# Optimization experiments

Measured on AMD Instinct MI355X. Metric: run time of the kernel, lower is better.

Reference implementation:

```python
import jax, jax.numpy as jnp
import numpy as np
import math

B, S, D = 16, 1024, 512
ALPHA = 1.0
DIRECTION = 'fw'


def masked_softmax(vec, mask):
    # faithful to the torch helper: multiply-by-mask, max-shift, exp, re-mask, normalize
    masked_vec = vec * mask
    max_vec = jnp.max(masked_vec, axis=2, keepdims=True)
    exps = jnp.exp(masked_vec - max_vec)
    masked_exps = exps * mask
    masked_sums = jnp.sum(masked_exps, axis=2, keepdims=True)
    masked_sums = masked_sums + (masked_sums == 0).astype(vec.dtype)
    return masked_exps / (masked_sums + 1e-20)


def setup_inputs() -> dict:
    key = jax.random.key(0)
    kq, kk, kv, km = jax.random.split(key, 4)
    q = jax.random.normal(kq, (B, S, D), dtype=jnp.float32)
    k = jax.random.normal(kk, (B, S, D), dtype=jnp.float32)
    v = jax.random.normal(kv, (B, S, D), dtype=jnp.float32)
    rep_mask = jax.random.randint(km, (B, S, 1), 0, 2, dtype=jnp.int32)
    return {"q": q, "k": k, "v": v, "rep_mask": rep_mask}


def reference(q, k, v, rep_mask):
    seq_len = q.shape[1]
    scale = jnp.asarray(math.sqrt(D), dtype=q.dtype)
    attention = jnp.einsum('bqd,bkd->bqk', q, k) / scale  # [B,S,S]

    ones = jnp.ones((seq_len, seq_len), dtype=q.dtype)
    if DIRECTION == 'fw':
        dir_mask = jnp.tril(ones, k=-1)
    else:
        dir_mask = jnp.triu(ones, k=1)

    rm = rep_mask.astype(q.dtype)                     # [B,S,1]
    rep = rm * jnp.swapaxes(rm, 1, 2)                 # [B,S,S]

    idx = jnp.arange(seq_len)
    dis_mask = -jnp.abs(idx[:, None] - idx[None, :]).astype(q.dtype)  # [S,S]

    mask = rep * dir_mask[None]                       # [B,S,S]
    attention = attention + ALPHA * dis_mask[None]
    attention = masked_softmax(attention, mask)
    out = jnp.einsum('bqk,bkd->bqd', attention, v)
    return (out, attention)
```

## Files before the change

kernel.cpp:

```cpp
#include <hip/hip_runtime.h>
#include <cstdint>

#define B_ 16
#define S_ 1024
#define D_ 512
#define TILE 128
#define BK 32
#define PITCH 36

typedef float f32x4 __attribute__((ext_vector_type(4)));
typedef short s16x8 __attribute__((ext_vector_type(8)));
typedef unsigned short u16;
typedef unsigned int u32;

__device__ __forceinline__ u16 f2bf(float f) {
    u32 u = __builtin_bit_cast(u32, f);
    u += 0x7FFFu + ((u >> 16) & 1u);
    return (u16)(u >> 16);
}

#define GLD16(g, l) __builtin_amdgcn_global_load_lds( \
    (const __attribute__((address_space(1))) u32*)(g), \
    (__attribute__((address_space(3))) u32*)(l), 16, 0, 0)

__global__ __launch_bounds__(256) void cvt_kernel(const float* __restrict__ src,
                                                  u16* __restrict__ dst) {
    int i = (blockIdx.x * 256 + threadIdx.x) * 8;
    float4 a = *(const float4*)(src + i);
    float4 b = *(const float4*)(src + i + 4);
    union { ushort4 h[2]; s16x8 v; } r;
    r.h[0] = make_ushort4(f2bf(a.x), f2bf(a.y), f2bf(a.z), f2bf(a.w));
    r.h[1] = make_ushort4(f2bf(b.x), f2bf(b.y), f2bf(b.z), f2bf(b.w));
    *(s16x8*)(dst + i) = r.v;
}

#define TP 66
__global__ __launch_bounds__(256) void trv_kernel(const float* __restrict__ v,
                                                  u16* __restrict__ vt) {
    const int d0 = blockIdx.x * 64, j0 = blockIdx.y * 64, b = blockIdx.z;
    __shared__ u16 t[64 * TP];
    const int tid = threadIdx.x;
    const int tj = tid >> 2;
    const int td = (tid & 3) * 16;
    const float* src = v + ((size_t)b * S_ + j0 + tj) * D_ + d0 + td;
#pragma unroll
    for (int e = 0; e < 4; ++e) {
        float4 a = *(const float4*)(src + e * 4);
        *(ushort4*)(t + tj * TP + td + e * 4) =
            make_ushort4(f2bf(a.x), f2bf(a.y), f2bf(a.z), f2bf(a.w));
    }
    __syncthreads();
    const int dd = tid >> 2;
    const int jj = (tid & 3) * 16;
    u16* dstp = vt + ((size_t)b * D_ + d0 + dd) * S_ + j0 + jj;
    u16 tmp[16];
#pragma unroll
    for (int e = 0; e < 16; ++e) tmp[e] = t[(jj + e) * TP + dd];
    *(s16x8*)dstp = *(s16x8*)tmp;
    *(s16x8*)(dstp + 8) = *(s16x8*)(tmp + 8);
}

__global__ __launch_bounds__(512, 2) void fused_qksm(const float* __restrict__ q,
                                                     const u16* __restrict__ Kb,
                                                     const int* __restrict__ rep,
                                                     float* __restrict__ attn) {
    const int bid = blockIdx.x;
    const int xcd = bid & 7, w = bid >> 3;
    const int b = xcd * 2 + (w & 1);
    const int qc = 31 - (w >> 1);
    const int i0 = qc * 32;
    const int ncolt = (qc >> 2) + 1;
    const int ncol = ncolt * 128;

    __shared__ u16 lQ[32 * 512];
    __shared__ u16 lK[1024 * 32];
    __shared__ int lrep[1024];
    __shared__ float lred[8][32][2];
    __shared__ float lrs[32][2];

    const int tid = threadIdx.x, lane = tid & 63, wid = tid >> 6;
    const int r15 = lane & 15, g4 = lane >> 4;

    {
        int2 rv = ((const int2*)(rep + (size_t)b * S_))[tid];
        lrep[tid * 2] = rv.x;
        lrep[tid * 2 + 1] = rv.y;
    }
    {
        const float* qg = q + ((size_t)b * S_ + i0) * D_;
#pragma unroll
        for (int e = 0; e < 4; ++e) {
            int G = e * 512 + tid;
            int i = G >> 6, c8 = G & 63;
            const float* src = qg + i * D_ + c8 * 8;
            float4 x0 = *(const float4*)src;
            float4 x1 = *(const float4*)(src + 4);
            union { ushort4 h[2]; s16x8 v; } rr;
            rr.h[0] = make_ushort4(f2bf(x0.x), f2bf(x0.y), f2bf(x0.z), f2bf(x0.w));
            rr.h[1] = make_ushort4(f2bf(x1.x), f2bf(x1.y), f2bf(x1.z), f2bf(x1.w));
            int unit = c8 ^ (i & 7);
            *(s16x8*)(lQ + i * 512 + unit * 8) = rr.v;
        }
    }
    __syncthreads();

    const u16* kbase = Kb + (size_t)b * S_ * D_;
    f32x4 acc[2][8] = {};

    for (int kk = 0; kk < 512; kk += 32) {
        for (int t = 0; t < ncolt; ++t) {
            int ud = t * 512 + tid;
            int p = ud >> 3, u = ud & 7;
            int lu = u ^ (p & 7);
            int j = p * 2 + (lu >> 2);
            int k16 = lu & 3;
            GLD16(kbase + (size_t)j * D_ + kk + k16 * 8, lK + t * 4096 + wid * 512);
        }
        __syncthreads();
        if (wid < ncolt) {
            s16x8 av[2], bv[8];
            int c8 = (kk >> 3) + g4;
#pragma unroll
            for (int rf = 0; rf < 2; ++rf) {
                int i = rf * 16 + r15;
                av[rf] = *(const s16x8*)(lQ + i * 512 + (c8 ^ (i & 7)) * 8);
            }
#pragma unroll
            for (int cf = 0; cf < 8; ++cf) {
                int j = wid * 128 + cf * 16 + r15;
                int p = j >> 1;
                int lu = (j & 1) * 4 + g4;
                bv[cf] = *(const s16x8*)(lK + p * 64 + (lu ^ (p & 7)) * 8);
            }
#pragma unroll
            for (int rf = 0; rf < 2; ++rf)
#pragma unroll
                for (int cf = 0; cf < 8; ++cf)
                    acc[rf][cf] = __builtin_amdgcn_mfma_f32_16x16x32_bf16(av[rf], bv[cf], acc[rf][cf], 0, 0, 0);
        }
        __syncthreads();
    }

    const float scale = 0.04419417382415922f;
    int mj[8];
#pragma unroll
    for (int cf = 0; cf < 8; ++cf) mj[cf] = lrep[wid * 128 + cf * 16 + r15];
    int mi_[2][4];
#pragma unroll
    for (int rf = 0; rf < 2; ++rf)
#pragma unroll
        for (int r = 0; r < 4; ++r) mi_[rf][r] = lrep[i0 + rf * 16 + g4 * 4 + r];

    float pm[2][4], ps[2][4];
#pragma unroll
    for (int rf = 0; rf < 2; ++rf)
#pragma unroll
        for (int r = 0; r < 4; ++r) {
            const int i = i0 + rf * 16 + g4 * 4 + r;
            const int im = mi_[rf][r];
            float m = 0.0f;
#pragma unroll
            for (int cf = 0; cf < 8; ++cf) {
                int j = wid * 128 + cf * 16 + r15;
                if (im && (j < i) && mj[cf])
                    m = fmaxf(m, acc[rf][cf][r] * scale - (float)(i - j));
            }
            float s = 0.0f;
#pragma unroll
            for (int cf = 0; cf < 8; ++cf) {
                int j = wid * 128 + cf * 16 + r15;
                if (im && (j < i) && mj[cf])
                    s += __expf(acc[rf][cf][r] * scale - (float)(i - j) - m);
            }
#pragma unroll
            for (int off = 1; off < 16; off <<= 1) {
                float om = __shfl_xor(m, off);
                float os = __shfl_xor(s, off);
                float M = fmaxf(m, om);
                s = s * __expf(m - M) + os * __expf(om - M);
                m = M;
            }
            pm[rf][r] = m;
            ps[rf][r] = s;
        }
    if (r15 == 0) {
#pragma unroll
        for (int rf = 0; rf < 2; ++rf)
#pragma unroll
            for (int r = 0; r < 4; ++r) {
                int rowl = rf * 16 + g4 * 4 + r;
                lred[wid][rowl][0] = pm[rf][r];
                lred[wid][rowl][1] = ps[rf][r];
            }
    }
    __syncthreads();
    if (tid < 32) {
        float M = 0.0f, S = 0.0f;
#pragma unroll
        for (int w2 = 0; w2 < 8; ++w2) M = fmaxf(M, lred[w2][tid][0]);
#pragma unroll
        for (int w2 = 0; w2 < 8; ++w2) S += lred[w2][tid][1] * __expf(lred[w2][tid][0] - M);
        float denom = (S == 0.0f ? 1.0f : S) + 1e-20f;
        lrs[tid][0] = M;
        lrs[tid][1] = 1.0f / denom;
    }
    __syncthreads();

    float* arow = attn + ((size_t)b * S_ + i0) * S_;
#pragma unroll
    for (int rf = 0; rf < 2; ++rf)
#pragma unroll
        for (int r = 0; r < 4; ++r) {
            const int il = rf * 16 + g4 * 4 + r;
            const int i = i0 + il;
            const int im = mi_[rf][r];
            const float M = lrs[il][0], inv = lrs[il][1];
#pragma unroll
            for (int cf = 0; cf < 8; ++cf) {
                int j = wid * 128 + cf * 16 + r15;
                float pv = 0.0f;
                if (im && (j < i) && mj[cf])
                    pv = __expf(acc[rf][cf][r] * scale - (float)(i - j) - M) * inv;
                arow[(size_t)il * S_ + j] = pv;
            }
        }
}

__device__ __forceinline__ s16x8 frag_swz(const u16* lds, int row, int colbyte) {
    int off = row * 128 + (colbyte ^ ((row & 7) << 4));
    return *(const s16x8*)((const char*)lds + off);
}

__global__ __launch_bounds__(256) void pv3_kernel(const float* __restrict__ attn,
                                                  const u16* __restrict__ Vt,
                                                  float* __restrict__ out) {
    const int bid = blockIdx.x;
    const int xcd = bid & 7, w = bid >> 3;
    const int b = xcd * 2 + (w & 1);
    const int r_ = w >> 1;
    const int dt = r_ & 3, qt = 7 - (r_ >> 2);

    __shared__ u16 lA[128 * 64];
    __shared__ u16 lB[128 * 64];
    const int tid = threadIdx.x, lane = tid & 63, wid = tid >> 6;
    const int l8 = lane >> 3, l7 = lane & 7;
    const int cswz = (l7 ^ l8) * 8;

    const float* ag = attn + ((size_t)b * S_ + (size_t)qt * 128) * S_;
    const u16* bg = Vt + ((size_t)b * D_ + (size_t)dt * 128) * S_;
    const u16* gb[4];
#pragma unroll
    for (int q2 = 0; q2 < 4; ++q2) {
        int seg = wid * 4 + q2;
        gb[q2] = bg + (size_t)(seg * 8 + l8) * S_ + cswz;
    }
    const int au = tid & 7;
    const int ar0 = (tid >> 3) * 4;

    f32x4 acc[4][4] = {};
    const int nk = (qt + 1) * 128;
    const int wr = (wid >> 1) * 64, wc = (wid & 1) * 64;
    const int r15 = lane & 15, cb = (lane >> 4) * 16;

    for (int kk = 0; kk < nk; kk += 64) {
#pragma unroll
        for (int q2 = 0; q2 < 4; ++q2)
            GLD16(gb[q2] + kk, lB + (wid * 4 + q2) * 512);
#pragma unroll
        for (int rr = 0; rr < 4; ++rr) {
            int row = ar0 + rr;
            const float* src = ag + (size_t)row * S_ + kk + au * 8;
            float4 x0 = *(const float4*)src;
            float4 x1 = *(const float4*)(src + 4);
            union { ushort4 h[2]; s16x8 v; } rv;
            rv.h[0] = make_ushort4(f2bf(x0.x), f2bf(x0.y), f2bf(x0.z), f2bf(x0.w));
            rv.h[1] = make_ushort4(f2bf(x1.x), f2bf(x1.y), f2bf(x1.z), f2bf(x1.w));
            *(s16x8*)(lA + row * 64 + (au ^ (row & 7)) * 8) = rv.v;
        }
        __syncthreads();
        s16x8 af[4], bf4[4];
#pragma unroll
        for (int ks = 0; ks < 2; ++ks) {
#pragma unroll
            for (int m = 0; m < 4; ++m) af[m] = frag_swz(lA, wr + m * 16 + r15, ks * 64 + cb);
#pragma unroll
            for (int n = 0; n < 4; ++n) bf4[n] = frag_swz(lB, wc + n * 16 + r15, ks * 64 + cb);
#pragma unroll
            for (int m = 0; m < 4; ++m)
#pragma unroll
                for (int n = 0; n < 4; ++n)
                    acc[m][n] = __builtin_amdgcn_mfma_f32_16x16x32_bf16(af[m], bf4[n], acc[m][n], 0, 0, 0);
        }
        __syncthreads();
    }

    size_t base = ((size_t)b * S_ + (size_t)qt * 128) * D_ + (size_t)dt * 128;
    const int rr2 = (lane >> 4) * 4;
#pragma unroll
    for (int m = 0; m < 4; ++m)
#pragma unroll
        for (int n = 0; n < 4; ++n)
#pragma unroll
            for (int r = 0; r < 4; ++r)
                out[base + (size_t)(wr + m * 16 + rr2 + r) * D_ + wc + n * 16 + r15] =
                    acc[m][n][r];
}


union Frag { s16x8 v; uint2 u[2]; };

__device__ __forceinline__ s16x8 load_frag(const u16* lds, int row, int kq) {
    Frag f;
    const u16* p = lds + row * PITCH + kq;
    f.u[0] = *(const uint2*)p;
    f.u[1] = *(const uint2*)(p + 4);
    return f.v;
}

__device__ __forceinline__ void stage_granule(u16* lds, const float* src, int ldsrc, int g) {
    int row = g >> 2;
    int c8 = (g & 3) * 8;
    const float4* s = (const float4*)(src + (size_t)row * ldsrc + c8);
    float4 x0 = s[0], x1 = s[1];
    *(ushort4*)(lds + row * PITCH + c8) =
        make_ushort4(f2bf(x0.x), f2bf(x0.y), f2bf(x0.z), f2bf(x0.w));
    *(ushort4*)(lds + row * PITCH + c8 + 4) =
        make_ushort4(f2bf(x1.x), f2bf(x1.y), f2bf(x1.z), f2bf(x1.w));
}

__global__ __launch_bounds__(256) void qk_kernel(const float* __restrict__ q,
                                                 const float* __restrict__ k,
                                                 float* __restrict__ attn) {
    const int kt = blockIdx.x, qt = blockIdx.y, b = blockIdx.z;
    if (kt > qt) return;
    __shared__ u16 lA[TILE * PITCH];
    __shared__ u16 lB[TILE * PITCH];
    const int tid = threadIdx.x;
    const int lane = tid & 63;
    const int wid = tid >> 6;
    const int wr = (wid >> 1) * 64, wc = (wid & 1) * 64;
    const int r15 = lane & 15, kq = (lane >> 4) * 8;
    const float* qb = q + ((size_t)b * S_ + (size_t)qt * TILE) * D_;
    const float* kb = k + ((size_t)b * S_ + (size_t)kt * TILE) * D_;
    f32x4 acc[4][4] = {};
    for (int kk = 0; kk < D_; kk += BK) {
        __syncthreads();
        stage_granule(lA, qb + kk, D_, tid);
        stage_granule(lA, qb + kk, D_, tid + 256);
        stage_granule(lB, kb + kk, D_, tid);
        stage_granule(lB, kb + kk, D_, tid + 256);
        __syncthreads();
        s16x8 af[4], bf[4];
#pragma unroll
        for (int m = 0; m < 4; ++m) af[m] = load_frag(lA, wr + m * 16 + r15, kq);
#pragma unroll
        for (int n = 0; n < 4; ++n) bf[n] = load_frag(lB, wc + n * 16 + r15, kq);
#pragma unroll
        for (int m = 0; m < 4; ++m)
#pragma unroll
            for (int n = 0; n < 4; ++n)
                acc[m][n] = __builtin_amdgcn_mfma_f32_16x16x32_bf16(af[m], bf[n], acc[m][n], 0, 0, 0);
    }
    const float scale = 0.04419417382415922f;
    size_t base = ((size_t)b * S_ + (size_t)qt * TILE) * S_ + (size_t)kt * TILE;
    const int rr = (lane >> 4) * 4;
#pragma unroll
    for (int m = 0; m < 4; ++m)
#pragma unroll
        for (int n = 0; n < 4; ++n)
#pragma unroll
            for (int r = 0; r < 4; ++r)
                attn[base + (size_t)(wr + m * 16 + rr + r) * S_ + wc + n * 16 + r15] =
                    acc[m][n][r] * scale;
}

__global__ __launch_bounds__(256) void sm_kernel(const int* __restrict__ rep_mask,
                                                 float* __restrict__ attn) {
    const int i = blockIdx.x, b = blockIdx.y;
    const int tid = threadIdx.x;
    const int lane = tid & 63, wid = tid >> 6;
    float* row = attn + ((size_t)b * S_ + i) * S_;
    const int* rm = rep_mask + (size_t)b * S_;
    __shared__ float red[8];
    const int mi = rm[i];
    const int j0 = tid * 4;
    int4 m4 = ((const int4*)rm)[tid];
    float4 lv = make_float4(0.f, 0.f, 0.f, 0.f);
    if (mi != 0 && j0 < i) lv = *(const float4*)(row + j0);
    const int mv[4] = {m4.x, m4.y, m4.z, m4.w};
    const float lf[4] = {lv.x, lv.y, lv.z, lv.w};
    float vec[4];
    bool val[4];
    float mymax = 0.0f;
#pragma unroll
    for (int e = 0; e < 4; ++e) {
        int j = j0 + e;
        val[e] = (mi != 0) && (j < i) && (mv[e] != 0);
        vec[e] = lf[e] - (float)(i - j);
        if (val[e]) mymax = fmaxf(mymax, vec[e]);
    }
#pragma unroll
    for (int off = 32; off > 0; off >>= 1) mymax = fmaxf(mymax, __shfl_down(mymax, off));
    if (lane == 0) red[wid] = mymax;
    __syncthreads();
    const float m = fmaxf(fmaxf(red[0], red[1]), fmaxf(red[2], red[3]));
    float ex[4];
    float mysum = 0.0f;
#pragma unroll
    for (int e = 0; e < 4; ++e) {
        ex[e] = val[e] ? expf(vec[e] - m) : 0.0f;
        mysum += ex[e];
    }
#pragma unroll
    for (int off = 32; off > 0; off >>= 1) mysum += __shfl_down(mysum, off);
    if (lane == 0) red[4 + wid] = mysum;
    __syncthreads();
    const float ssum = red[4] + red[5] + red[6] + red[7];
    const float denom = ssum + (ssum == 0.0f ? 1.0f : 0.0f) + 1e-20f;
    const float inv = 1.0f / denom;
    *(float4*)(row + j0) = make_float4(ex[0] * inv, ex[1] * inv, ex[2] * inv, ex[3] * inv);
}

__global__ __launch_bounds__(256) void pv_kernel(const float* __restrict__ attn,
                                                 const float* __restrict__ v,
                                                 float* __restrict__ out) {
    const int dt = blockIdx.x, qt = blockIdx.y, b = blockIdx.z;
    __shared__ u16 lP[TILE * PITCH];
    __shared__ u16 lV[TILE * PITCH];
    const int tid = threadIdx.x;
    const int lane = tid & 63;
    const int wid = tid >> 6;
    const int wr = (wid >> 1) * 64, wc = (wid & 1) * 64;
    const int r15 = lane & 15, kq = (lane >> 4) * 8;
    const float* pb = attn + ((size_t)b * S_ + (size_t)qt * TILE) * S_;
    const float* vb = v + (size_t)b * S_ * D_ + (size_t)dt * TILE;
    const int vd0 = (tid & 31) * 4;
    const int vj0 = (tid >> 5) * 4;
    f32x4 acc[4][4] = {};
    const int nk = (qt + 1) * TILE;
    for (int kk = 0; kk < nk; kk += BK) {
        __syncthreads();
        stage_granule(lP, pb + kk, S_, tid);
        stage_granule(lP, pb + kk, S_, tid + 256);
        {
            const float* vs = vb + (size_t)(kk + vj0) * D_ + vd0;
            float4 r0 = *(const float4*)vs;
            float4 r1 = *(const float4*)(vs + D_);
            float4 r2 = *(const float4*)(vs + 2 * D_);
            float4 r3 = *(const float4*)(vs + 3 * D_);
            *(ushort4*)(lV + (vd0 + 0) * PITCH + vj0) = make_ushort4(f2bf(r0.x), f2bf(r1.x), f2bf(r2.x), f2bf(r3.x));
            *(ushort4*)(lV + (vd0 + 1) * PITCH + vj0) = make_ushort4(f2bf(r0.y), f2bf(r1.y), f2bf(r2.y), f2bf(r3.y));
            *(ushort4*)(lV + (vd0 + 2) * PITCH + vj0) = make_ushort4(f2bf(r0.z), f2bf(r1.z), f2bf(r2.z), f2bf(r3.z));
            *(ushort4*)(lV + (vd0 + 3) * PITCH + vj0) = make_ushort4(f2bf(r0.w), f2bf(r1.w), f2bf(r2.w), f2bf(r3.w));
        }
        __syncthreads();
        s16x8 af[4], bf[4];
#pragma unroll
        for (int m = 0; m < 4; ++m) af[m] = load_frag(lP, wr + m * 16 + r15, kq);
#pragma unroll
        for (int n = 0; n < 4; ++n) bf[n] = load_frag(lV, wc + n * 16 + r15, kq);
#pragma unroll
        for (int m = 0; m < 4; ++m)
#pragma unroll
            for (int n = 0; n < 4; ++n)
                acc[m][n] = __builtin_amdgcn_mfma_f32_16x16x32_bf16(af[m], bf[n], acc[m][n], 0, 0, 0);
    }
    size_t base = ((size_t)b * S_ + (size_t)qt * TILE) * D_ + (size_t)dt * TILE;
    const int rr = (lane >> 4) * 4;
#pragma unroll
    for (int m = 0; m < 4; ++m)
#pragma unroll
        for (int n = 0; n < 4; ++n)
#pragma unroll
            for (int r = 0; r < 4; ++r)
                out[base + (size_t)(wr + m * 16 + rr + r) * D_ + wc + n * 16 + r15] =
                    acc[m][n][r];
}

extern "C" void kernel_launch(void* const* d_in, const int* in_sizes, int n_in,
                              void* d_out, int out_size, void* d_ws, size_t ws_size,
                              hipStream_t stream) {
    const float* q = (const float*)d_in[0];
    const float* k = (const float*)d_in[1];
    const float* v = (const float*)d_in[2];
    const int* rep = (const int*)d_in[3];
    float* out = (float*)d_out;
    float* attn = out + (size_t)B_ * S_ * D_;

    const size_t nqk = (size_t)B_ * S_ * D_;
    const size_t need = 2 * nqk * sizeof(u16);
    if (ws_size >= need) {
        u16* Kb = (u16*)d_ws;
        u16* Vt = Kb + nqk;
        cvt_kernel<<<nqk / (8 * 256), 256, 0, stream>>>(k, Kb);
        trv_kernel<<<dim3(D_ / 64, S_ / 64, B_), 256, 0, stream>>>(v, Vt);
        fused_qksm<<<512, 512, 0, stream>>>(q, Kb, rep, attn);
        pv3_kernel<<<512, 256, 0, stream>>>(attn, Vt, out);
    } else {
        qk_kernel<<<dim3(S_ / TILE, S_ / TILE, B_), 256, 0, stream>>>(q, k, attn);
        sm_kernel<<<dim3(S_, B_), 256, 0, stream>>>(rep, attn);
        pv_kernel<<<dim3(D_ / TILE, S_ / TILE, B_), 256, 0, stream>>>(attn, v, out);
    }
}
```

Measured before the change: 105.9 us.

## Load K directly from global, interleave column tiles, and emit bf16 P for PV

```diff
diff --git a/kernel.cpp b/kernel.cpp
--- a/kernel.cpp
+++ b/kernel.cpp
@@ -60,20 +60,19 @@
     *(s16x8*)(dstp + 8) = *(s16x8*)(tmp + 8);
 }
 
-__global__ __launch_bounds__(512, 2) void fused_qksm(const float* __restrict__ q,
-                                                     const u16* __restrict__ Kb,
-                                                     const int* __restrict__ rep,
-                                                     float* __restrict__ attn) {
+__global__ __launch_bounds__(512, 4) void qksm2(const float* __restrict__ q,
+                                                const u16* __restrict__ Kb,
+                                                const int* __restrict__ rep,
+                                                float* __restrict__ attn,
+                                                u16* __restrict__ Pb) {
     const int bid = blockIdx.x;
     const int xcd = bid & 7, w = bid >> 3;
     const int b = xcd * 2 + (w & 1);
     const int qc = 31 - (w >> 1);
     const int i0 = qc * 32;
     const int ncolt = (qc >> 2) + 1;
-    const int ncol = ncolt * 128;
 
     __shared__ u16 lQ[32 * 512];
-    __shared__ u16 lK[1024 * 32];
     __shared__ int lrep[1024];
     __shared__ float lred[8][32][2];
     __shared__ float lrs[32][2];
@@ -104,47 +103,36 @@
     }
     __syncthreads();
 
-    const u16* kbase = Kb + (size_t)b * S_ * D_;
+    const u16* kbu = Kb + (size_t)b * S_ * D_ + g4 * 8;
+    int koff[8];
+#pragma unroll
+    for (int cf = 0; cf < 8; ++cf)
+        koff[cf] = ((wid + 8 * cf) * 16 + r15) * D_;
+
     f32x4 acc[2][8] = {};
-
     for (int kk = 0; kk < 512; kk += 32) {
-        for (int t = 0; t < ncolt; ++t) {
-            int ud = t * 512 + tid;
-            int p = ud >> 3, u = ud & 7;
-            int lu = u ^ (p & 7);
-            int j = p * 2 + (lu >> 2);
-            int k16 = lu & 3;
-            GLD16(kbase + (size_t)j * D_ + kk + k16 * 8, lK + t * 4096 + wid * 512);
-        }
-        __syncthreads();
-        if (wid < ncolt) {
-            s16x8 av[2], bv[8];
-            int c8 = (kk >> 3) + g4;
-#pragma unroll
-            for (int rf = 0; rf < 2; ++rf) {
-                int i = rf * 16 + r15;
-                av[rf] = *(const s16x8*)(lQ + i * 512 + (c8 ^ (i & 7)) * 8);
+        int c8 = (kk >> 3) + g4;
+        s16x8 av0, av1;
+        {
+            int i = r15;
+            av0 = *(const s16x8*)(lQ + i * 512 + (c8 ^ (i & 7)) * 8);
+            i = 16 + r15;
+            av1 = *(const s16x8*)(lQ + i * 512 + (c8 ^ (i & 7)) * 8);
+        }
+#pragma unroll
+        for (int cf = 0; cf < 8; ++cf) {
+            if (cf < ncolt) {
+                s16x8 bv = *(const s16x8*)(kbu + koff[cf] + kk);
+                acc[0][cf] = __builtin_amdgcn_mfma_f32_16x16x32_bf16(av0, bv, acc[0][cf], 0, 0, 0);
+                acc[1][cf] = __builtin_amdgcn_mfma_f32_16x16x32_bf16(av1, bv, acc[1][cf], 0, 0, 0);
             }
-#pragma unroll
-            for (int cf = 0; cf < 8; ++cf) {
-                int j = wid * 128 + cf * 16 + r15;
-                int p = j >> 1;
-                int lu = (j & 1) * 4 + g4;
-                bv[cf] = *(const s16x8*)(lK + p * 64 + (lu ^ (p & 7)) * 8);
-            }
-#pragma unroll
-            for (int rf = 0; rf < 2; ++rf)
-#pragma unroll
-                for (int cf = 0; cf < 8; ++cf)
-                    acc[rf][cf] = __builtin_amdgcn_mfma_f32_16x16x32_bf16(av[rf], bv[cf], acc[rf][cf], 0, 0, 0);
-        }
-        __syncthreads();
+        }
     }
 
     const float scale = 0.04419417382415922f;
     int mj[8];
 #pragma unroll
-    for (int cf = 0; cf < 8; ++cf) mj[cf] = lrep[wid * 128 + cf * 16 + r15];
+    for (int cf = 0; cf < 8; ++cf) mj[cf] = lrep[(wid + 8 * cf) * 16 + r15];
     int mi_[2][4];
 #pragma unroll
     for (int rf = 0; rf < 2; ++rf)
@@ -161,14 +149,14 @@
             float m = 0.0f;
 #pragma unroll
             for (int cf = 0; cf < 8; ++cf) {
-                int j = wid * 128 + cf * 16 + r15;
+                int j = (wid + 8 * cf) * 16 + r15;
                 if (im && (j < i) && mj[cf])
                     m = fmaxf(m, acc[rf][cf][r] * scale - (float)(i - j));
             }
             float s = 0.0f;
 #pragma unroll
             for (int cf = 0; cf < 8; ++cf) {
-                int j = wid * 128 + cf * 16 + r15;
+                int j = (wid + 8 * cf) * 16 + r15;
                 if (im && (j < i) && mj[cf])
                     s += __expf(acc[rf][cf][r] * scale - (float)(i - j) - m);
             }
@@ -207,6 +195,7 @@
     __syncthreads();
 
     float* arow = attn + ((size_t)b * S_ + i0) * S_;
+    u16* prow = Pb ? Pb + ((size_t)b * S_ + i0) * S_ : nullptr;
 #pragma unroll
     for (int rf = 0; rf < 2; ++rf)
 #pragma unroll
@@ -217,11 +206,13 @@
             const float M = lrs[il][0], inv = lrs[il][1];
 #pragma unroll
             for (int cf = 0; cf < 8; ++cf) {
-                int j = wid * 128 + cf * 16 + r15;
+                int j = (wid + 8 * cf) * 16 + r15;
                 float pv = 0.0f;
                 if (im && (j < i) && mj[cf])
                     pv = __expf(acc[rf][cf][r] * scale - (float)(i - j) - M) * inv;
                 arow[(size_t)il * S_ + j] = pv;
+                if (prow && cf < ncolt)
+                    prow[(size_t)il * S_ + j] = f2bf(pv);
             }
         }
 }
@@ -229,6 +220,80 @@
 __device__ __forceinline__ s16x8 frag_swz(const u16* lds, int row, int colbyte) {
     int off = row * 128 + (colbyte ^ ((row & 7) << 4));
     return *(const s16x8*)((const char*)lds + off);
+}
+
+__device__ __forceinline__ void gemm_body(const u16* ag, const u16* bg, int lda, int ldb,
+                                          int nk, u16* lA, u16* lB, f32x4 acc[4][4],
+                                          int tid) {
+    const int lane = tid & 63, wid = tid >> 6;
+    const int l8 = lane >> 3, l7 = lane & 7;
+    const int cswz = (l7 ^ l8) * 8;
+    const u16* ga[4];
+    const u16* gb[4];
+#pragma unroll
+    for (int q2 = 0; q2 < 4; ++q2) {
+        int seg = wid * 4 + q2;
+        int row = seg * 8 + l8;
+        ga[q2] = ag + (size_t)row * lda + cswz;
+        gb[q2] = bg + (size_t)row * ldb + cswz;
+    }
+    const int wr = (wid >> 1) * 64, wc = (wid & 1) * 64;
+    const int r15 = lane & 15;
+    const int cb = (lane >> 4) * 16;
+
+    for (int kk = 0; kk < nk; kk += 64) {
+#pragma unroll
+        for (int q2 = 0; q2 < 4; ++q2) {
+            int seg = wid * 4 + q2;
+            GLD16(ga[q2] + kk, lA + seg * 512);
+            GLD16(gb[q2] + kk, lB + seg * 512);
+        }
+        __syncthreads();
+#pragma unroll
+        for (int ks = 0; ks < 2; ++ks) {
+            s16x8 af[4], bf4[4];
+#pragma unroll
+            for (int m = 0; m < 4; ++m) af[m] = frag_swz(lA, wr + m * 16 + r15, ks * 64 + cb);
+#pragma unroll
+            for (int n = 0; n < 4; ++n) bf4[n] = frag_swz(lB, wc + n * 16 + r15, ks * 64 + cb);
+#pragma unroll
+            for (int m = 0; m < 4; ++m)
+#pragma unroll
+                for (int n = 0; n < 4; ++n)
+                    acc[m][n] = __builtin_amdgcn_mfma_f32_16x16x32_bf16(af[m], bf4[n], acc[m][n], 0, 0, 0);
+        }
+        __syncthreads();
+    }
+}
+
+__global__ __launch_bounds__(256) void pv2_kernel(const u16* __restrict__ Pb,
+                                                  const u16* __restrict__ Vt,
+                                                  float* __restrict__ out) {
+    const int bid = blockIdx.x;
+    const int xcd = bid & 7;
+    const int w = bid >> 3;
+    const int b = xcd * 2 + (w & 1);
+    const int r = w >> 1;
+    const int dt = r & 3, qt = 7 - (r >> 2);
+
+    __shared__ u16 lA[128 * 64];
+    __shared__ u16 lB[128 * 64];
+    const int tid = threadIdx.x, lane = tid & 63, wid = tid >> 6;
+    f32x4 acc[4][4] = {};
+    gemm_body(Pb + ((size_t)b * S_ + (size_t)qt * 128) * S_,
+              Vt + ((size_t)b * D_ + (size_t)dt * 128) * S_,
+              S_, S_, (qt + 1) * 128, lA, lB, acc, tid);
+    const int wr = (wid >> 1) * 64, wc = (wid & 1) * 64;
+    const int r15 = lane & 15, rr = (lane >> 4) * 4;
+    size_t base = ((size_t)b * S_ + (size_t)qt * 128) * D_ + (size_t)dt * 128;
+#pragma unroll
+    for (int m = 0; m < 4; ++m)
+#pragma unroll
+        for (int n = 0; n < 4; ++n)
+#pragma unroll
+            for (int rg = 0; rg < 4; ++rg)
+                out[base + (size_t)(wr + m * 16 + rr + rg) * D_ + wc + n * 16 + r15] =
+                    acc[m][n][rg];
 }
 
 __global__ __launch_bounds__(256) void pv3_kernel(const float* __restrict__ attn,
@@ -488,14 +553,21 @@
     float* attn = out + (size_t)B_ * S_ * D_;
 
     const size_t nqk = (size_t)B_ * S_ * D_;
-    const size_t need = 2 * nqk * sizeof(u16);
-    if (ws_size >= need) {
+    const size_t nss = (size_t)B_ * S_ * S_;
+    const size_t need_small = 2 * nqk * sizeof(u16);
+    const size_t need_big = (2 * nqk + nss) * sizeof(u16);
+
+    if (ws_size >= need_small) {
         u16* Kb = (u16*)d_ws;
         u16* Vt = Kb + nqk;
+        u16* Pb = (ws_size >= need_big) ? (Vt + nqk) : nullptr;
         cvt_kernel<<<nqk / (8 * 256), 256, 0, stream>>>(k, Kb);
         trv_kernel<<<dim3(D_ / 64, S_ / 64, B_), 256, 0, stream>>>(v, Vt);
-        fused_qksm<<<512, 512, 0, stream>>>(q, Kb, rep, attn);
-        pv3_kernel<<<512, 256, 0, stream>>>(attn, Vt, out);
+        qksm2<<<512, 512, 0, stream>>>(q, Kb, rep, attn, Pb);
+        if (Pb)
+            pv2_kernel<<<512, 256, 0, stream>>>(Pb, Vt, out);
+        else
+            pv3_kernel<<<512, 256, 0, stream>>>(attn, Vt, out);
     } else {
         qk_kernel<<<dim3(S_ / TILE, S_ / TILE, B_), 256, 0, stream>>>(q, k, attn);
         sm_kernel<<<dim3(S_, B_), 256, 0, stream>>>(rep, attn);
```

Result: slower. 109.8 us (+3.6%).

## Fuse PV matmul into QK-softmax kernel and load K directly to registers

Applied to the files above, without the earlier changes.

```diff
diff --git a/kernel.cpp b/kernel.cpp
--- a/kernel.cpp
+++ b/kernel.cpp
@@ -18,10 +18,6 @@
     u += 0x7FFFu + ((u >> 16) & 1u);
     return (u16)(u >> 16);
 }
-
-#define GLD16(g, l) __builtin_amdgcn_global_load_lds( \
-    (const __attribute__((address_space(1))) u32*)(g), \
-    (__attribute__((address_space(3))) u32*)(l), 16, 0, 0)
 
 __global__ __launch_bounds__(256) void cvt_kernel(const float* __restrict__ src,
                                                   u16* __restrict__ dst) {
@@ -60,10 +56,18 @@
     *(s16x8*)(dstp + 8) = *(s16x8*)(tmp + 8);
 }
 
-__global__ __launch_bounds__(512, 2) void fused_qksm(const float* __restrict__ q,
-                                                     const u16* __restrict__ Kb,
-                                                     const int* __restrict__ rep,
-                                                     float* __restrict__ attn) {
+__device__ __forceinline__ int plds_off(int row, int col) {
+    int u = col >> 3;
+    int e = col & 7;
+    return row * 128 + (((u ^ (row & 15)) << 3) | e);
+}
+
+__global__ __launch_bounds__(512, 2) void qksm3(const float* __restrict__ q,
+                                                const u16* __restrict__ Kb,
+                                                const u16* __restrict__ Vt,
+                                                const int* __restrict__ rep,
+                                                float* __restrict__ attn,
+                                                float* __restrict__ out) {
     const int bid = blockIdx.x;
     const int xcd = bid & 7, w = bid >> 3;
     const int b = xcd * 2 + (w & 1);
@@ -73,7 +77,7 @@
     const int ncol = ncolt * 128;
 
     __shared__ u16 lQ[32 * 512];
-    __shared__ u16 lK[1024 * 32];
+    __shared__ u16 lP[32 * 128];
     __shared__ int lrep[1024];
     __shared__ float lred[8][32][2];
     __shared__ float lrs[32][2];
@@ -104,47 +108,32 @@
     }
     __syncthreads();
 
-    const u16* kbase = Kb + (size_t)b * S_ * D_;
+    const u16* kbu = Kb + (size_t)b * S_ * D_ + g4 * 8;
     f32x4 acc[2][8] = {};
-
-    for (int kk = 0; kk < 512; kk += 32) {
-        for (int t = 0; t < ncolt; ++t) {
-            int ud = t * 512 + tid;
-            int p = ud >> 3, u = ud & 7;
-            int lu = u ^ (p & 7);
-            int j = p * 2 + (lu >> 2);
-            int k16 = lu & 3;
-            GLD16(kbase + (size_t)j * D_ + kk + k16 * 8, lK + t * 4096 + wid * 512);
+#pragma unroll
+    for (int cf = 0; cf < 8; ++cf) {
+        if (cf < ncolt) {
+            const u16* kp = kbu + (size_t)((wid + 8 * cf) * 16 + r15) * D_;
+            s16x8 bv[16];
+#pragma unroll
+            for (int g = 0; g < 16; ++g) bv[g] = *(const s16x8*)(kp + g * 32);
+#pragma unroll
+            for (int g = 0; g < 16; ++g) {
+                int c8 = g * 4 + g4;
+                int i = r15;
+                s16x8 av0 = *(const s16x8*)(lQ + i * 512 + (c8 ^ (i & 7)) * 8);
+                i = 16 + r15;
+                s16x8 av1 = *(const s16x8*)(lQ + i * 512 + (c8 ^ (i & 7)) * 8);
+                acc[0][cf] = __builtin_amdgcn_mfma_f32_16x16x32_bf16(av0, bv[g], acc[0][cf], 0, 0, 0);
+                acc[1][cf] = __builtin_amdgcn_mfma_f32_16x16x32_bf16(av1, bv[g], acc[1][cf], 0, 0, 0);
+            }
         }
-        __syncthreads();
-        if (wid < ncolt) {
-            s16x8 av[2], bv[8];
-            int c8 = (kk >> 3) + g4;
-#pragma unroll
-            for (int rf = 0; rf < 2; ++rf) {
-                int i = rf * 16 + r15;
-                av[rf] = *(const s16x8*)(lQ + i * 512 + (c8 ^ (i & 7)) * 8);
-            }
-#pragma unroll
-            for (int cf = 0; cf < 8; ++cf) {
-                int j = wid * 128 + cf * 16 + r15;
-                int p = j >> 1;
-                int lu = (j & 1) * 4 + g4;
-                bv[cf] = *(const s16x8*)(lK + p * 64 + (lu ^ (p & 7)) * 8);
-            }
-#pragma unroll
-            for (int rf = 0; rf < 2; ++rf)
-#pragma unroll
-                for (int cf = 0; cf < 8; ++cf)
-                    acc[rf][cf] = __builtin_amdgcn_mfma_f32_16x16x32_bf16(av[rf], bv[cf], acc[rf][cf], 0, 0, 0);
-        }
-        __syncthreads();
     }
 
     const float scale = 0.04419417382415922f;
     int mj[8];
 #pragma unroll
-    for (int cf = 0; cf < 8; ++cf) mj[cf] = lrep[wid * 128 + cf * 16 + r15];
+    for (int cf = 0; cf < 8; ++cf) mj[cf] = lrep[(wid + 8 * cf) * 16 + r15];
     int mi_[2][4];
 #pragma unroll
     for (int rf = 0; rf < 2; ++rf)
@@ -161,14 +150,14 @@
             float m = 0.0f;
 #pragma unroll
             for (int cf = 0; cf < 8; ++cf) {
-                int j = wid * 128 + cf * 16 + r15;
+                int j = (wid + 8 * cf) * 16 + r15;
                 if (im && (j < i) && mj[cf])
                     m = fmaxf(m, acc[rf][cf][r] * scale - (float)(i - j));
             }
             float s = 0.0f;
 #pragma unroll
             for (int cf = 0; cf < 8; ++cf) {
-                int j = wid * 128 + cf * 16 + r15;
+                int j = (wid + 8 * cf) * 16 + r15;
                 if (im && (j < i) && mj[cf])
                     s += __expf(acc[rf][cf][r] * scale - (float)(i - j) - m);
             }
@@ -207,103 +196,68 @@
     __syncthreads();
 
     float* arow = attn + ((size_t)b * S_ + i0) * S_;
+
+    {
+        int zrow = tid >> 4;
+        for (int c = ncol + (tid & 15) * 4; c < S_; c += 64)
+            *(float4*)(arow + (size_t)zrow * S_ + c) = make_float4(0.f, 0.f, 0.f, 0.f);
+    }
+
+    const u16* vtb = Vt + (size_t)b * D_ * S_ + g4 * 8;
+    f32x4 oacc[2][4] = {};
+#pragma unroll
+    for (int c = 0; c < 8; ++c) {
+        if (c < ncolt) {
+            s16x8 vbv[16];
+#pragma unroll
+            for (int kg = 0; kg < 4; ++kg)
+#pragma unroll
+                for (int nf = 0; nf < 4; ++nf)
+                    vbv[kg * 4 + nf] = *(const s16x8*)(vtb +
+                        (size_t)(wid * 64 + nf * 16 + r15) * S_ + c * 128 + kg * 32);
+            __syncthreads();
+#pragma unroll
+            for (int rf = 0; rf < 2; ++rf)
+#pragma unroll
+                for (int r = 0; r < 4; ++r) {
+                    const int il = rf * 16 + g4 * 4 + r;
+                    const int i = i0 + il;
+                    const int im = mi_[rf][r];
+                    const float M = lrs[il][0], inv = lrs[il][1];
+                    const int jc = wid * 16 + r15;
+                    const int j = c * 128 + jc;
+                    float pv = 0.0f;
+                    if (im && (j < i) && mj[c])
+                        pv = __expf(acc[rf][c][r] * scale - (float)(i - j) - M) * inv;
+                    arow[(size_t)il * S_ + j] = pv;
+                    lP[plds_off(il, jc)] = f2bf(pv);
+                }
+            __syncthreads();
+#pragma unroll
+            for (int kg = 0; kg < 4; ++kg) {
+                s16x8 pa[2];
+#pragma unroll
+                for (int rf = 0; rf < 2; ++rf)
+                    pa[rf] = *(const s16x8*)(lP + plds_off(rf * 16 + r15, kg * 32 + g4 * 8));
+#pragma unroll
+                for (int rf = 0; rf < 2; ++rf)
+#pragma unroll
+                    for (int nf = 0; nf < 4; ++nf)
+                        oacc[rf][nf] = __builtin_amdgcn_mfma_f32_16x16x32_bf16(
+                            pa[rf], vbv[kg * 4 + nf], oacc[rf][nf], 0, 0, 0);
+            }
+        }
+    }
+
+    float* obase = out + ((size_t)b * S_ + i0) * D_;
 #pragma unroll
     for (int rf = 0; rf < 2; ++rf)
 #pragma unroll
-        for (int r = 0; r < 4; ++r) {
-            const int il = rf * 16 + g4 * 4 + r;
-            const int i = i0 + il;
-            const int im = mi_[rf][r];
-            const float M = lrs[il][0], inv = lrs[il][1];
-#pragma unroll
-            for (int cf = 0; cf < 8; ++cf) {
-                int j = wid * 128 + cf * 16 + r15;
-                float pv = 0.0f;
-                if (im && (j < i) && mj[cf])
-                    pv = __expf(acc[rf][cf][r] * scale - (float)(i - j) - M) * inv;
-                arow[(size_t)il * S_ + j] = pv;
-            }
-        }
-}
-
-__device__ __forceinline__ s16x8 frag_swz(const u16* lds, int row, int colbyte) {
-    int off = row * 128 + (colbyte ^ ((row & 7) << 4));
-    return *(const s16x8*)((const char*)lds + off);
-}
-
-__global__ __launch_bounds__(256) void pv3_kernel(const float* __restrict__ attn,
-                                                  const u16* __restrict__ Vt,
-                                                  float* __restrict__ out) {
-    const int bid = blockIdx.x;
-    const int xcd = bid & 7, w = bid >> 3;
-    const int b = xcd * 2 + (w & 1);
-    const int r_ = w >> 1;
-    const int dt = r_ & 3, qt = 7 - (r_ >> 2);
-
-    __shared__ u16 lA[128 * 64];
-    __shared__ u16 lB[128 * 64];
-    const int tid = threadIdx.x, lane = tid & 63, wid = tid >> 6;
-    const int l8 = lane >> 3, l7 = lane & 7;
-    const int cswz = (l7 ^ l8) * 8;
-
-    const float* ag = attn + ((size_t)b * S_ + (size_t)qt * 128) * S_;
-    const u16* bg = Vt + ((size_t)b * D_ + (size_t)dt * 128) * S_;
-    const u16* gb[4];
-#pragma unroll
-    for (int q2 = 0; q2 < 4; ++q2) {
-        int seg = wid * 4 + q2;
-        gb[q2] = bg + (size_t)(seg * 8 + l8) * S_ + cswz;
-    }
-    const int au = tid & 7;
-    const int ar0 = (tid >> 3) * 4;
-
-    f32x4 acc[4][4] = {};
-    const int nk = (qt + 1) * 128;
-    const int wr = (wid >> 1) * 64, wc = (wid & 1) * 64;
-    const int r15 = lane & 15, cb = (lane >> 4) * 16;
-
-    for (int kk = 0; kk < nk; kk += 64) {
-#pragma unroll
-        for (int q2 = 0; q2 < 4; ++q2)
-            GLD16(gb[q2] + kk, lB + (wid * 4 + q2) * 512);
-#pragma unroll
-        for (int rr = 0; rr < 4; ++rr) {
-            int row = ar0 + rr;
-            const float* src = ag + (size_t)row * S_ + kk + au * 8;
-            float4 x0 = *(const float4*)src;
-            float4 x1 = *(const float4*)(src + 4);
-            union { ushort4 h[2]; s16x8 v; } rv;
-            rv.h[0] = make_ushort4(f2bf(x0.x), f2bf(x0.y), f2bf(x0.z), f2bf(x0.w));
-            rv.h[1] = make_ushort4(f2bf(x1.x), f2bf(x1.y), f2bf(x1.z), f2bf(x1.w));
-            *(s16x8*)(lA + row * 64 + (au ^ (row & 7)) * 8) = rv.v;
-        }
-        __syncthreads();
-        s16x8 af[4], bf4[4];
-#pragma unroll
-        for (int ks = 0; ks < 2; ++ks) {
-#pragma unroll
-            for (int m = 0; m < 4; ++m) af[m] = frag_swz(lA, wr + m * 16 + r15, ks * 64 + cb);
-#pragma unroll
-            for (int n = 0; n < 4; ++n) bf4[n] = frag_swz(lB, wc + n * 16 + r15, ks * 64 + cb);
-#pragma unroll
-            for (int m = 0; m < 4; ++m)
-#pragma unroll
-                for (int n = 0; n < 4; ++n)
-                    acc[m][n] = __builtin_amdgcn_mfma_f32_16x16x32_bf16(af[m], bf4[n], acc[m][n], 0, 0, 0);
-        }
-        __syncthreads();
-    }
-
-    size_t base = ((size_t)b * S_ + (size_t)qt * 128) * D_ + (size_t)dt * 128;
-    const int rr2 = (lane >> 4) * 4;
-#pragma unroll
-    for (int m = 0; m < 4; ++m)
-#pragma unroll
-        for (int n = 0; n < 4; ++n)
-#pragma unroll
-            for (int r = 0; r < 4; ++r)
-                out[base + (size_t)(wr + m * 16 + rr2 + r) * D_ + wc + n * 16 + r15] =
-                    acc[m][n][r];
+        for (int nf = 0; nf < 4; ++nf)
+#pragma unroll
+            for (int rg = 0; rg < 4; ++rg)
+                obase[(size_t)(rf * 16 + g4 * 4 + rg) * D_ + wid * 64 + nf * 16 + r15] =
+                    oacc[rf][nf][rg];
 }
 
 
@@ -494,8 +448,7 @@
         u16* Vt = Kb + nqk;
         cvt_kernel<<<nqk / (8 * 256), 256, 0, stream>>>(k, Kb);
         trv_kernel<<<dim3(D_ / 64, S_ / 64, B_), 256, 0, stream>>>(v, Vt);
-        fused_qksm<<<512, 512, 0, stream>>>(q, Kb, rep, attn);
-        pv3_kernel<<<512, 256, 0, stream>>>(attn, Vt, out);
+        qksm3<<<512, 512, 0, stream>>>(q, Kb, Vt, rep, attn, out);
     } else {
         qk_kernel<<<dim3(S_ / TILE, S_ / TILE, B_), 256, 0, stream>>>(q, k, attn);
         sm_kernel<<<dim3(S_, B_), 256, 0, stream>>>(rep, attn);
```

After: 117.4 us. +10.9%, slower.
